# Kernel optimization log

Hardware: AMD Instinct MI355X
Metric: run time of the kernel (lower is better)

Reference implementation:

```python
import jax, jax.numpy as jnp
import numpy as np

N_HEADS = 8


def setup_inputs() -> dict:
    key = jax.random.key(0)
    qkv = jax.random.normal(key, (4, 1536, 2048), dtype=jnp.float32)
    return {"qkv": qkv}


def reference(qkv):
    bs, width, length = qkv.shape
    assert width % (3 * N_HEADS) == 0
    ch = width // (3 * N_HEADS)
    q, k, v = jnp.split(qkv, 3, axis=1)            # each [bs, H*C, T]
    scale = 1.0 / (ch ** 0.25)                      # 1/sqrt(sqrt(ch)) applied to both q and k
    q = (q * scale).reshape(bs * N_HEADS, ch, length)
    k = (k * scale).reshape(bs * N_HEADS, ch, length)
    v = v.reshape(bs * N_HEADS, ch, length)
    weight = jnp.einsum('bct,bcs->bts', q, k)       # [bs*H, T, T]
    weight = jax.nn.softmax(weight.astype(jnp.float32), axis=-1).astype(weight.dtype)
    a = jnp.einsum('bts,bcs->bct', weight, v)       # [bs*H, C, T]
    return a.reshape(bs, -1, length)
```

## Files before the change

### kernel.cpp

```cpp
#include <hip/hip_runtime.h>


typedef _Float16 half8  __attribute__((ext_vector_type(8)));
typedef _Float16 half4  __attribute__((ext_vector_type(4)));
typedef float    floatx4 __attribute__((ext_vector_type(4)));

constexpr int T    = 2048;
constexpr int TQ   = 128;
constexpr int TS   = 64;
constexpr int LDK  = 72;
constexpr int LDV  = 72;
constexpr int KHALF  = TS * LDK;
constexpr int SMEM_H = KHALF + 64 * LDV;
constexpr int NIT  = T / TS;
constexpr float QSCALE = 0.125f * 1.44269504088896340736f;

__device__ __forceinline__ half4 pack4(float a, float b, float c, float d) {
    half4 r;
    r[0] = (_Float16)a; r[1] = (_Float16)b;
    r[2] = (_Float16)c; r[3] = (_Float16)d;
    return r;
}

__global__ __launch_bounds__(512, 4)
void qkv_attn_kernel(const float* __restrict__ qkv, float* __restrict__ out) {
    __shared__ __align__(16) _Float16 smem[2][SMEM_H];

    const int tid  = threadIdx.x;
    const int wave = tid >> 6;
    const int lane = tid & 63;
    const int n16  = lane & 15;
    const int g    = lane >> 4;
    const int h    = wave >> 2;
    const int qg   = wave & 3;

    const int bx = blockIdx.x;
    const int hd = bx & 31;
    const int qt = bx >> 5;
    const int b  = hd >> 3;
    const int hh = hd & 7;
    const int q0 = qt * TQ;

    const float* __restrict__ qbase = qkv + (size_t)(b * 1536 + hh * 64) * T;
    const float* __restrict__ kbase = qkv + (size_t)(b * 1536 + 512 + hh * 64) * T;
    const float* __restrict__ vbase = qkv + (size_t)(b * 1536 + 1024 + hh * 64) * T;
    float* __restrict__ obase = out + (size_t)(b * 512 + hh * 64) * T;

    const bool kstage = (wave < 4);
    const int ptid = tid & 255;
    const int ks   = ((ptid >> 6) << 4) | (ptid & 15);
    const int kc4  = ((ptid >> 4) & 3) << 2;
    const int vc   = ptid >> 4;
    const int vt   = ptid & 15;
    const int vcol = 32 * (vt >> 3) + 8 * (vt & 3) + 4 * ((vt >> 2) & 1);

    float pre[16];
    auto prefetch = [&](int s0) {
        if (kstage) {
            const float* kg = kbase + s0 + ks;
#pragma unroll
            for (int i = 0; i < 4; ++i) {
                const int c = i * 16 + kc4;
#pragma unroll
                for (int j = 0; j < 4; ++j) pre[i * 4 + j] = kg[(c + j) * T];
            }
        } else {
            const float* vg = vbase + vc * T + s0 + vt * 4;
#pragma unroll
            for (int i = 0; i < 4; ++i) {
                const floatx4 vv = *(const floatx4*)&vg[i * 16 * T];
                pre[i * 4 + 0] = vv.x; pre[i * 4 + 1] = vv.y;
                pre[i * 4 + 2] = vv.z; pre[i * 4 + 3] = vv.w;
            }
        }
    };
    auto flush = [&](int buf) {
        if (kstage) {
            _Float16* kd = &smem[buf][ks * LDK];
#pragma unroll
            for (int i = 0; i < 4; ++i)
                *(half4*)&kd[i * 16 + kc4] =
                    pack4(pre[i * 4], pre[i * 4 + 1], pre[i * 4 + 2], pre[i * 4 + 3]);
        } else {
            _Float16* vd = &smem[buf][KHALF + vc * LDV + vcol];
#pragma unroll
            for (int i = 0; i < 4; ++i)
                *(half4*)&vd[i * 16 * LDV] =
                    pack4(pre[i * 4], pre[i * 4 + 1], pre[i * 4 + 2], pre[i * 4 + 3]);
        }
    };

    half8 bq[2][2];
    floatx4 oacc[4][2];
    floatx4 lacc[2];
    half8 aone;
#pragma unroll
    for (int i = 0; i < 8; ++i) aone[i] = (_Float16)1.f;

#pragma unroll
    for (int qt2 = 0; qt2 < 2; ++qt2) {
        const int q = q0 + qg * 32 + qt2 * 16 + n16;
#pragma unroll
        for (int kcA = 0; kcA < 2; ++kcA)
#pragma unroll
            for (int j = 0; j < 8; ++j) {
                const int c = kcA * 32 + g * 8 + j;
                bq[qt2][kcA][j] = (_Float16)(qbase[c * T + q] * QSCALE);
            }
    }
#pragma unroll
    for (int mt = 0; mt < 4; ++mt)
#pragma unroll
        for (int qt2 = 0; qt2 < 2; ++qt2) oacc[mt][qt2] = (floatx4)(0.f);
    lacc[0] = (floatx4)(0.f);
    lacc[1] = (floatx4)(0.f);

    prefetch(0);
    flush(0);
    __syncthreads();

    for (int it = 0; it < NIT; ++it) {
        const int buf = it & 1;
        if (it + 1 < NIT) prefetch((it + 1) * TS);

        const _Float16* kb = &smem[buf][0];
        const _Float16* vb = &smem[buf][KHALF];

        floatx4 sacc[2][2];
#pragma unroll
        for (int sub = 0; sub < 2; ++sub) {
            const half8 ak0 = *(const half8*)&kb[((h * 2 + sub) * 16 + n16) * LDK + g * 8];
            const half8 ak1 = *(const half8*)&kb[((h * 2 + sub) * 16 + n16) * LDK + 32 + g * 8];
            __builtin_amdgcn_s_setprio(1);
#pragma unroll
            for (int qt2 = 0; qt2 < 2; ++qt2) {
                floatx4 acc = (floatx4)(0.f);
                acc = __builtin_amdgcn_mfma_f32_16x16x32_f16(ak0, bq[qt2][0], acc, 0, 0, 0);
                acc = __builtin_amdgcn_mfma_f32_16x16x32_f16(ak1, bq[qt2][1], acc, 0, 0, 0);
                sacc[qt2][sub] = acc;
            }
            __builtin_amdgcn_s_setprio(0);
        }
        half8 av[4];
#pragma unroll
        for (int mt = 0; mt < 4; ++mt)
            av[mt] = *(const half8*)&vb[(mt * 16 + n16) * LDV + h * 32 + g * 8];
#pragma unroll
        for (int qt2 = 0; qt2 < 2; ++qt2) {
            float pv[8];
#pragma unroll
            for (int sub = 0; sub < 2; ++sub)
#pragma unroll
                for (int r = 0; r < 4; ++r)
                    pv[sub * 4 + r] = __builtin_amdgcn_exp2f(sacc[qt2][sub][r]);
            half8 bp;
#pragma unroll
            for (int i = 0; i < 8; ++i) bp[i] = (_Float16)pv[i];
            __builtin_amdgcn_s_setprio(1);
#pragma unroll
            for (int mt = 0; mt < 4; ++mt)
                oacc[mt][qt2] = __builtin_amdgcn_mfma_f32_16x16x32_f16(
                    av[mt], bp, oacc[mt][qt2], 0, 0, 0);
            lacc[qt2] = __builtin_amdgcn_mfma_f32_16x16x32_f16(
                aone, bp, lacc[qt2], 0, 0, 0);
            __builtin_amdgcn_s_setprio(0);
        }

        if (it + 1 < NIT) flush(buf ^ 1);
        __syncthreads();
    }

    float* red = (float*)&smem[0][0];
    const int rbase = (qg * 64 + lane) * 36;
    if (h == 1) {
#pragma unroll
        for (int qt2 = 0; qt2 < 2; ++qt2)
#pragma unroll
            for (int mt = 0; mt < 4; ++mt)
                *(floatx4*)&red[rbase + (qt2 * 4 + mt) * 4] = oacc[mt][qt2];
        red[rbase + 32] = lacc[0][0];
        red[rbase + 33] = lacc[1][0];
    }
    __syncthreads();
    if (h == 0) {
#pragma unroll
        for (int qt2 = 0; qt2 < 2; ++qt2)
#pragma unroll
            for (int mt = 0; mt < 4; ++mt)
                oacc[mt][qt2] += *(const floatx4*)&red[rbase + (qt2 * 4 + mt) * 4];
#pragma unroll
        for (int qt2 = 0; qt2 < 2; ++qt2) {
            const float l = lacc[qt2][0] + red[rbase + 32 + qt2];
            const float linv = 1.0f / l;
            const int tcol = q0 + qg * 32 + qt2 * 16 + n16;
#pragma unroll
            for (int mt = 0; mt < 4; ++mt)
#pragma unroll
                for (int r = 0; r < 4; ++r)
                    obase[(mt * 16 + g * 4 + r) * T + tcol] = oacc[mt][qt2][r] * linv;
        }
    }
}

extern "C" void kernel_launch(void* const* d_in, const int* in_sizes, int n_in,
                              void* d_out, int out_size, void* d_ws, size_t ws_size,
                              hipStream_t stream) {
    const float* qkv = (const float*)d_in[0];
    float* out = (float*)d_out;
    qkv_attn_kernel<<<dim3(512), dim3(512), 0, stream>>>(qkv, out);
}
```

Measured before the change: 121.9 us.

## Double the key/value tile per iteration to halve barriers and loop trips

Each loop iteration now stages 128 key/value positions instead of 64, so the number of block-wide barriers and loop trips is halved. Each wave processes two 64-column chunks, and the LDS flush of the next tile is split into two halves interleaved with the compute chunks. The cost is double the prefetch registers (32 floats) and a larger shared-memory footprint per block, which may lower occupancy under the 512x4 launch bound.

```diff
diff --git a/kernel.cpp b/kernel.cpp
--- a/kernel.cpp
+++ b/kernel.cpp
@@ -7,12 +7,12 @@
 
 constexpr int T    = 2048;
 constexpr int TQ   = 128;
-constexpr int TS   = 64;
+constexpr int BT   = 128;
 constexpr int LDK  = 72;
-constexpr int LDV  = 72;
-constexpr int KHALF  = TS * LDK;
+constexpr int LDV  = 136;
+constexpr int KHALF  = BT * LDK;
 constexpr int SMEM_H = KHALF + 64 * LDV;
-constexpr int NIT  = T / TS;
+constexpr int NIT  = T / BT;
 constexpr float QSCALE = 0.125f * 1.44269504088896340736f;
 
 __device__ __forceinline__ half4 pack4(float a, float b, float c, float d) {
@@ -54,39 +54,45 @@
     const int vt   = ptid & 15;
     const int vcol = 32 * (vt >> 3) + 8 * (vt & 3) + 4 * ((vt >> 2) & 1);
 
-    float pre[16];
+    float pre[32];
     auto prefetch = [&](int s0) {
+#pragma unroll
+        for (int u = 0; u < 2; ++u) {
+            if (kstage) {
+                const float* kg = kbase + s0 + u * 64 + ks;
+#pragma unroll
+                for (int i = 0; i < 4; ++i) {
+                    const int c = i * 16 + kc4;
+#pragma unroll
+                    for (int j = 0; j < 4; ++j)
+                        pre[u * 16 + i * 4 + j] = kg[(c + j) * T];
+                }
+            } else {
+                const float* vg = vbase + vc * T + s0 + u * 64 + vt * 4;
+#pragma unroll
+                for (int i = 0; i < 4; ++i) {
+                    const floatx4 vv = *(const floatx4*)&vg[i * 16 * T];
+                    pre[u * 16 + i * 4 + 0] = vv.x; pre[u * 16 + i * 4 + 1] = vv.y;
+                    pre[u * 16 + i * 4 + 2] = vv.z; pre[u * 16 + i * 4 + 3] = vv.w;
+                }
+            }
+        }
+    };
+    auto flush = [&](int buf, int u) {
         if (kstage) {
-            const float* kg = kbase + s0 + ks;
-#pragma unroll
-            for (int i = 0; i < 4; ++i) {
-                const int c = i * 16 + kc4;
-#pragma unroll
-                for (int j = 0; j < 4; ++j) pre[i * 4 + j] = kg[(c + j) * T];
-            }
-        } else {
-            const float* vg = vbase + vc * T + s0 + vt * 4;
-#pragma unroll
-            for (int i = 0; i < 4; ++i) {
-                const floatx4 vv = *(const floatx4*)&vg[i * 16 * T];
-                pre[i * 4 + 0] = vv.x; pre[i * 4 + 1] = vv.y;
-                pre[i * 4 + 2] = vv.z; pre[i * 4 + 3] = vv.w;
-            }
-        }
-    };
-    auto flush = [&](int buf) {
-        if (kstage) {
-            _Float16* kd = &smem[buf][ks * LDK];
+            _Float16* kd = &smem[buf][(u * 64 + ks) * LDK];
 #pragma unroll
             for (int i = 0; i < 4; ++i)
                 *(half4*)&kd[i * 16 + kc4] =
-                    pack4(pre[i * 4], pre[i * 4 + 1], pre[i * 4 + 2], pre[i * 4 + 3]);
+                    pack4(pre[u * 16 + i * 4], pre[u * 16 + i * 4 + 1],
+                          pre[u * 16 + i * 4 + 2], pre[u * 16 + i * 4 + 3]);
         } else {
-            _Float16* vd = &smem[buf][KHALF + vc * LDV + vcol];
+            _Float16* vd = &smem[buf][KHALF + vc * LDV + u * 64 + vcol];
 #pragma unroll
             for (int i = 0; i < 4; ++i)
                 *(half4*)&vd[i * 16 * LDV] =
-                    pack4(pre[i * 4], pre[i * 4 + 1], pre[i * 4 + 2], pre[i * 4 + 3]);
+                    pack4(pre[u * 16 + i * 4], pre[u * 16 + i * 4 + 1],
+                          pre[u * 16 + i * 4 + 2], pre[u * 16 + i * 4 + 3]);
         }
     };
 
@@ -116,57 +122,66 @@
     lacc[1] = (floatx4)(0.f);
 
     prefetch(0);
-    flush(0);
+    flush(0, 0);
+    flush(0, 1);
     __syncthreads();
 
     for (int it = 0; it < NIT; ++it) {
         const int buf = it & 1;
-        if (it + 1 < NIT) prefetch((it + 1) * TS);
+        if (it + 1 < NIT) prefetch((it + 1) * BT);
 
         const _Float16* kb = &smem[buf][0];
         const _Float16* vb = &smem[buf][KHALF];
 
-        floatx4 sacc[2][2];
-#pragma unroll
-        for (int sub = 0; sub < 2; ++sub) {
-            const half8 ak0 = *(const half8*)&kb[((h * 2 + sub) * 16 + n16) * LDK + g * 8];
-            const half8 ak1 = *(const half8*)&kb[((h * 2 + sub) * 16 + n16) * LDK + 32 + g * 8];
-            __builtin_amdgcn_s_setprio(1);
+        floatx4 sacc[2][2][2];
+#pragma unroll
+        for (int c = 0; c < 2; ++c) {
+#pragma unroll
+            for (int sub = 0; sub < 2; ++sub) {
+                const int srow = (4 * h + 2 * c + sub) * 16 + n16;
+                const half8 ak0 = *(const half8*)&kb[srow * LDK + g * 8];
+                const half8 ak1 = *(const half8*)&kb[srow * LDK + 32 + g * 8];
+                __builtin_amdgcn_s_setprio(1);
+#pragma unroll
+                for (int qt2 = 0; qt2 < 2; ++qt2) {
+                    floatx4 acc = (floatx4)(0.f);
+                    acc = __builtin_amdgcn_mfma_f32_16x16x32_f16(ak0, bq[qt2][0], acc, 0, 0, 0);
+                    acc = __builtin_amdgcn_mfma_f32_16x16x32_f16(ak1, bq[qt2][1], acc, 0, 0, 0);
+                    sacc[c][qt2][sub] = acc;
+                }
+                __builtin_amdgcn_s_setprio(0);
+            }
+        }
+
+#pragma unroll
+        for (int c = 0; c < 2; ++c) {
+            half8 av[4];
+#pragma unroll
+            for (int mt = 0; mt < 4; ++mt)
+                av[mt] = *(const half8*)&vb[(mt * 16 + n16) * LDV + h * 64 + c * 32 + g * 8];
 #pragma unroll
             for (int qt2 = 0; qt2 < 2; ++qt2) {
-                floatx4 acc = (floatx4)(0.f);
-                acc = __builtin_amdgcn_mfma_f32_16x16x32_f16(ak0, bq[qt2][0], acc, 0, 0, 0);
-                acc = __builtin_amdgcn_mfma_f32_16x16x32_f16(ak1, bq[qt2][1], acc, 0, 0, 0);
-                sacc[qt2][sub] = acc;
-            }
-            __builtin_amdgcn_s_setprio(0);
-        }
-        half8 av[4];
-#pragma unroll
-        for (int mt = 0; mt < 4; ++mt)
-            av[mt] = *(const half8*)&vb[(mt * 16 + n16) * LDV + h * 32 + g * 8];
-#pragma unroll
-        for (int qt2 = 0; qt2 < 2; ++qt2) {
-            float pv[8];
-#pragma unroll
-            for (int sub = 0; sub < 2; ++sub)
-#pragma unroll
-                for (int r = 0; r < 4; ++r)
-                    pv[sub * 4 + r] = __builtin_amdgcn_exp2f(sacc[qt2][sub][r]);
-            half8 bp;
-#pragma unroll
-            for (int i = 0; i < 8; ++i) bp[i] = (_Float16)pv[i];
-            __builtin_amdgcn_s_setprio(1);
-#pragma unroll
-            for (int mt = 0; mt < 4; ++mt)
-                oacc[mt][qt2] = __builtin_amdgcn_mfma_f32_16x16x32_f16(
-                    av[mt], bp, oacc[mt][qt2], 0, 0, 0);
-            lacc[qt2] = __builtin_amdgcn_mfma_f32_16x16x32_f16(
-                aone, bp, lacc[qt2], 0, 0, 0);
-            __builtin_amdgcn_s_setprio(0);
-        }
-
-        if (it + 1 < NIT) flush(buf ^ 1);
+                float pv[8];
+#pragma unroll
+                for (int sub = 0; sub < 2; ++sub)
+#pragma unroll
+                    for (int r = 0; r < 4; ++r)
+                        pv[sub * 4 + r] = __builtin_amdgcn_exp2f(sacc[c][qt2][sub][r]);
+                half8 bp;
+#pragma unroll
+                for (int i = 0; i < 8; ++i) bp[i] = (_Float16)pv[i];
+                __builtin_amdgcn_s_setprio(1);
+#pragma unroll
+                for (int mt = 0; mt < 4; ++mt)
+                    oacc[mt][qt2] = __builtin_amdgcn_mfma_f32_16x16x32_f16(
+                        av[mt], bp, oacc[mt][qt2], 0, 0, 0);
+                lacc[qt2] = __builtin_amdgcn_mfma_f32_16x16x32_f16(
+                    aone, bp, lacc[qt2], 0, 0, 0);
+                __builtin_amdgcn_s_setprio(0);
+            }
+            if (it + 1 < NIT) flush(buf ^ 1, c);
+        }
+
         __syncthreads();
     }
 
```

New measurement: 188.9 us. 55.0% more time.
